# Kernel tuning notes

Measured on AMD Instinct MI355X. Metric: run time of the kernel, lower is better.

## Reference

```python
import jax, jax.numpy as jnp
import numpy as np

B, N_KERNELS, IN_DIM, UNITS = 512, 128, 1024, 1024

def setup_inputs() -> dict:
    key = jax.random.key(0)
    k1, k2 = jax.random.split(key)
    x = jax.random.normal(k1, (B, N_KERNELS, IN_DIM), dtype=jnp.float32)
    kernels = jax.random.normal(k2, (N_KERNELS, IN_DIM, UNITS), dtype=jnp.float32) * 0.02
    return {"x": x, "kernels": kernels}

def reference(x, kernels):
    # Original loops over n_kernels doing x[:, i:i+1, :] @ kernels[i] then softplus.
    # Note: the original's K.bias_add return value is discarded, so bias never
    # affects the output; the faithful math has no bias term.
    # Batched GEMM over the position axis k: [B,K,I] x [K,I,O] -> [B,K,O]
    out = jax.nn.softplus(jnp.einsum('bki,kio->bko', x, kernels))
    return out
```

## Files before the change

### kernel.cpp

```cpp
#include <hip/hip_runtime.h>

#define NKER  128
#define INDIM 1024
#define UNITS 1024

typedef __attribute__((ext_vector_type(8)))  short          bf16x8;
typedef __attribute__((ext_vector_type(4)))  float          f32x4;
typedef __attribute__((ext_vector_type(4)))  unsigned short u16x4;
typedef __attribute__((ext_vector_type(8)))  unsigned short u16x8;

__device__ __forceinline__ unsigned short f2bf(float f) {
    return __builtin_bit_cast(unsigned short, static_cast<__bf16>(f));
}

__device__ __forceinline__ int swzidx(int r, int k) {
    return r * 32 + ((((k >> 3) ^ ((r >> 1) & 3)) << 3) | (k & 7));
}

__global__ void __launch_bounds__(256, 2)
dense_local(const float* __restrict__ X, const float* __restrict__ Kn,
            float* __restrict__ Out)
{
    __shared__ __align__(16) unsigned short lA[2][128 * 32];
    __shared__ __align__(16) unsigned short lB[2][128 * 32];

    const int bid  = blockIdx.x;
    const int wg   = (bid & 7) * 512 + (bid >> 3);
    const int kidx = wg >> 5;
    const int tile = wg & 31;
    const int mt   = tile >> 3;
    const int nt   = tile & 7;

    const int t  = threadIdx.x;
    const int l  = t & 63;
    const int w  = t >> 6;
    const int wr = w >> 1, wc = w & 1;
    const int l15 = l & 15, g = l >> 4;

    const size_t MROW = (size_t)NKER * INDIM;

    const float* Abase = X  + (size_t)mt * 128 * MROW + (size_t)kidx * INDIM;
    const float* Bbase = Kn + (size_t)kidx * INDIM * UNITS + nt * 128;
    float*       Cbase = Out + (size_t)mt * 128 * MROW + (size_t)kidx * UNITS + nt * 128;

    const int ar0 = t >> 3;
    const int akq = (t & 7) << 2;
    const int bn  = ((w & 1) << 6) | l;
    const int bkh = w >> 1;

    f32x4 acc[4][4];
#pragma unroll
    for (int mi = 0; mi < 4; ++mi)
#pragma unroll
        for (int ni = 0; ni < 4; ++ni)
            acc[mi][ni] = f32x4{0.f, 0.f, 0.f, 0.f};

    f32x4 av[4];
    float bv[16];

    auto loadg = [&](int kc) {
#pragma unroll
        for (int p = 0; p < 4; ++p)
            av[p] = *(const f32x4*)(Abase + (size_t)(ar0 + p * 32) * MROW + kc + akq);
        const float* bp = Bbase + (size_t)(kc + bkh * 16) * UNITS + bn;
#pragma unroll
        for (int j = 0; j < 16; ++j)
            bv[j] = bp[(size_t)j * UNITS];
    };

    auto writes = [&](int bb) {
#pragma unroll
        for (int p = 0; p < 4; ++p) {
            const int row = ar0 + p * 32;
            u16x4 h;
#pragma unroll
            for (int c = 0; c < 4; ++c) h[c] = f2bf(av[p][c]);
            *(u16x4*)&lA[bb][swzidx(row, akq)] = h;
        }
        u16x8 h0, h1;
#pragma unroll
        for (int j = 0; j < 8; ++j) { h0[j] = f2bf(bv[j]); h1[j] = f2bf(bv[j + 8]); }
        *(u16x8*)&lB[bb][swzidx(bn, bkh * 16)]     = h0;
        *(u16x8*)&lB[bb][swzidx(bn, bkh * 16 + 8)] = h1;
    };

    auto compute = [&](int bb) {
        bf16x8 af[4], bfr[4];
#pragma unroll
        for (int mi = 0; mi < 4; ++mi) {
            const int r = wr * 64 + mi * 16 + l15;
            af[mi] = *(const bf16x8*)&lA[bb][swzidx(r, g * 8)];
        }
#pragma unroll
        for (int ni = 0; ni < 4; ++ni) {
            const int r = wc * 64 + ni * 16 + l15;
            bfr[ni] = *(const bf16x8*)&lB[bb][swzidx(r, g * 8)];
        }
#pragma unroll
        for (int mi = 0; mi < 4; ++mi)
#pragma unroll
            for (int ni = 0; ni < 4; ++ni)
                acc[mi][ni] = __builtin_amdgcn_mfma_f32_16x16x32_bf16(
                    af[mi], bfr[ni], acc[mi][ni], 0, 0, 0);
    };

    loadg(0);
    writes(0);
    __syncthreads();

    int bb = 0;
#pragma unroll 1
    for (int step = 0; step < 32; ++step) {
        if (step < 31) loadg((step + 1) * 32);
        compute(bb);
        __syncthreads();
        if (step < 31) writes(bb ^ 1);
        __syncthreads();
        bb ^= 1;
    }

#pragma unroll
    for (int mi = 0; mi < 4; ++mi) {
#pragma unroll
        for (int ni = 0; ni < 4; ++ni) {
            const int n = wc * 64 + ni * 16 + l15;
#pragma unroll
            for (int r = 0; r < 4; ++r) {
                const int m = wr * 64 + mi * 16 + g * 4 + r;
                const float v  = acc[mi][ni][r];
                const float sp = fmaxf(v, 0.0f) + log1pf(__expf(-fabsf(v)));
                Cbase[(size_t)m * MROW + n] = sp;
            }
        }
    }
}

extern "C" void kernel_launch(void* const* d_in, const int* in_sizes, int n_in,
                              void* d_out, int out_size, void* d_ws, size_t ws_size,
                              hipStream_t stream) {
    const float* X  = (const float*)d_in[0];
    const float* Kn = (const float*)d_in[1];
    float* O = (float*)d_out;
    dense_local<<<4096, 256, 0, stream>>>(X, Kn, O);
}
```

Measured before the change: 408.0 us.

## Stream A tile to LDS via direct global_load_lds and convert at fragment read

The fp32 A tile now goes straight from global memory into LDS with global_load_lds (XOR-swizzled by column group). It is converted to bf16 only when fragments are read, so register staging and the convert-and-store pass for A disappear. B conversion uses a cheaper rounding pack via perm, and the main loop is unrolled by two with one barrier per half. It also raises launch bounds to 3 waves-per-SIMD occupancy and adds setprio around the MFMA block. The trade-off is doubled LDS for A (fp32 storage) and extra conversion ALU in the compute phase, with possible occupancy limits from LDS size.

```diff
diff --git a/kernel.cpp b/kernel.cpp
--- a/kernel.cpp
+++ b/kernel.cpp
@@ -4,25 +4,31 @@
 #define INDIM 1024
 #define UNITS 1024
 
-typedef __attribute__((ext_vector_type(8)))  short          bf16x8;
-typedef __attribute__((ext_vector_type(4)))  float          f32x4;
-typedef __attribute__((ext_vector_type(4)))  unsigned short u16x4;
-typedef __attribute__((ext_vector_type(8)))  unsigned short u16x8;
+typedef __attribute__((ext_vector_type(8))) short          bf16x8;
+typedef __attribute__((ext_vector_type(4))) float          f32x4;
+typedef __attribute__((ext_vector_type(4))) unsigned int   u32x4;
 
-__device__ __forceinline__ unsigned short f2bf(float f) {
-    return __builtin_bit_cast(unsigned short, static_cast<__bf16>(f));
+typedef __attribute__((address_space(1))) const unsigned int gas_t;
+typedef __attribute__((address_space(3)))       unsigned int las_t;
+#define GLOAD16(g, l) \
+    __builtin_amdgcn_global_load_lds((gas_t*)(g), (las_t*)(l), 16, 0, 0)
+
+__device__ __forceinline__ unsigned int bpack2(float lo, float hi) {
+    unsigned int ul = __builtin_bit_cast(unsigned int, lo) + 0x8000u;
+    unsigned int uh = __builtin_bit_cast(unsigned int, hi) + 0x8000u;
+    return __builtin_amdgcn_perm(uh, ul, 0x07060302u);
 }
 
 __device__ __forceinline__ int swzidx(int r, int k) {
     return r * 32 + ((((k >> 3) ^ ((r >> 1) & 3)) << 3) | (k & 7));
 }
 
-__global__ void __launch_bounds__(256, 2)
+__global__ void __launch_bounds__(256, 3)
 dense_local(const float* __restrict__ X, const float* __restrict__ Kn,
             float* __restrict__ Out)
 {
-    __shared__ __align__(16) unsigned short lA[2][128 * 32];
-    __shared__ __align__(16) unsigned short lB[2][128 * 32];
+    __shared__ __align__(16) float          lAf[2][128 * 32];
+    __shared__ __align__(16) unsigned short lB [2][128 * 32];
 
     const int bid  = blockIdx.x;
     const int wg   = (bid & 7) * 512 + (bid >> 3);
@@ -31,22 +37,26 @@
     const int mt   = tile >> 3;
     const int nt   = tile & 7;
 
-    const int t  = threadIdx.x;
-    const int l  = t & 63;
-    const int w  = t >> 6;
-    const int wr = w >> 1, wc = w & 1;
+    const int t   = threadIdx.x;
+    const int l   = t & 63;
+    const int w   = t >> 6;
+    const int wr  = w >> 1, wc = w & 1;
     const int l15 = l & 15, g = l >> 4;
 
     const size_t MROW = (size_t)NKER * INDIM;
 
-    const float* Abase = X  + (size_t)mt * 128 * MROW + (size_t)kidx * INDIM;
-    const float* Bbase = Kn + (size_t)kidx * INDIM * UNITS + nt * 128;
+    const float* Abase = X   + (size_t)mt * 128 * MROW + (size_t)kidx * INDIM;
+    const float* Bbase = Kn  + (size_t)kidx * INDIM * UNITS + nt * 128;
     float*       Cbase = Out + (size_t)mt * 128 * MROW + (size_t)kidx * UNITS + nt * 128;
 
-    const int ar0 = t >> 3;
-    const int akq = (t & 7) << 2;
+    const int  rlo  = (t >> 3) & 7;
+    const int  cgl  = (t & 7) ^ rlo;
+    const float* aG = Abase + (size_t)(w * 32 + rlo) * MROW + cgl * 4;
+    const size_t MR8 = (size_t)8 * MROW;
+
     const int bn  = ((w & 1) << 6) | l;
     const int bkh = w >> 1;
+    const float* bG = Bbase + (size_t)(bkh * 16) * UNITS + bn;
 
     f32x4 acc[4][4];
 #pragma unroll
@@ -55,68 +65,72 @@
         for (int ni = 0; ni < 4; ++ni)
             acc[mi][ni] = f32x4{0.f, 0.f, 0.f, 0.f};
 
-    f32x4 av[4];
     float bv[16];
 
-    auto loadg = [&](int kc) {
-#pragma unroll
-        for (int p = 0; p < 4; ++p)
-            av[p] = *(const f32x4*)(Abase + (size_t)(ar0 + p * 32) * MROW + kc + akq);
-        const float* bp = Bbase + (size_t)(kc + bkh * 16) * UNITS + bn;
+    auto gloadA = [&](int nb) {
+        GLOAD16(aG,            &lAf[nb][(w * 4 + 0) * 256]);
+        GLOAD16(aG + MR8,      &lAf[nb][(w * 4 + 1) * 256]);
+        GLOAD16(aG + 2 * MR8,  &lAf[nb][(w * 4 + 2) * 256]);
+        GLOAD16(aG + 3 * MR8,  &lAf[nb][(w * 4 + 3) * 256]);
+        aG += 32;
+    };
+    auto loadB = [&]() {
 #pragma unroll
         for (int j = 0; j < 16; ++j)
-            bv[j] = bp[(size_t)j * UNITS];
+            bv[j] = bG[(size_t)j * UNITS];
+        bG += (size_t)32 * UNITS;
+    };
+    auto writeB = [&](int nb) {
+        u32x4 W0{bpack2(bv[0], bv[1]),  bpack2(bv[2], bv[3]),
+                 bpack2(bv[4], bv[5]),  bpack2(bv[6], bv[7])};
+        u32x4 W1{bpack2(bv[8], bv[9]),  bpack2(bv[10], bv[11]),
+                 bpack2(bv[12], bv[13]), bpack2(bv[14], bv[15])};
+        *(u32x4*)&lB[nb][swzidx(bn, bkh * 16)]     = W0;
+        *(u32x4*)&lB[nb][swzidx(bn, bkh * 16 + 8)] = W1;
     };
 
-    auto writes = [&](int bb) {
-#pragma unroll
-        for (int p = 0; p < 4; ++p) {
-            const int row = ar0 + p * 32;
-            u16x4 h;
-#pragma unroll
-            for (int c = 0; c < 4; ++c) h[c] = f2bf(av[p][c]);
-            *(u16x4*)&lA[bb][swzidx(row, akq)] = h;
-        }
-        u16x8 h0, h1;
-#pragma unroll
-        for (int j = 0; j < 8; ++j) { h0[j] = f2bf(bv[j]); h1[j] = f2bf(bv[j + 8]); }
-        *(u16x8*)&lB[bb][swzidx(bn, bkh * 16)]     = h0;
-        *(u16x8*)&lB[bb][swzidx(bn, bkh * 16 + 8)] = h1;
-    };
-
-    auto compute = [&](int bb) {
+    auto compute = [&](int c) {
         bf16x8 af[4], bfr[4];
 #pragma unroll
         for (int mi = 0; mi < 4; ++mi) {
-            const int r = wr * 64 + mi * 16 + l15;
-            af[mi] = *(const bf16x8*)&lA[bb][swzidx(r, g * 8)];
+            const int arow = wr * 64 + mi * 16 + l15;
+            const int ax   = l15 & 7;
+            const float* pa = &lAf[c][arow * 32];
+            f32x4 v0 = *(const f32x4*)(pa + ((( 2 * g)      ^ ax) << 2));
+            f32x4 v1 = *(const f32x4*)(pa + (((2 * g + 1)   ^ ax) << 2));
+            u32x4 pw{bpack2(v0[0], v0[1]), bpack2(v0[2], v0[3]),
+                     bpack2(v1[0], v1[1]), bpack2(v1[2], v1[3])};
+            af[mi] = __builtin_bit_cast(bf16x8, pw);
         }
 #pragma unroll
-        for (int ni = 0; ni < 4; ++ni) {
-            const int r = wc * 64 + ni * 16 + l15;
-            bfr[ni] = *(const bf16x8*)&lB[bb][swzidx(r, g * 8)];
-        }
+        for (int ni = 0; ni < 4; ++ni)
+            bfr[ni] = *(const bf16x8*)&lB[c][swzidx(wc * 64 + ni * 16 + l15, g * 8)];
+        __builtin_amdgcn_s_setprio(1);
 #pragma unroll
         for (int mi = 0; mi < 4; ++mi)
 #pragma unroll
             for (int ni = 0; ni < 4; ++ni)
                 acc[mi][ni] = __builtin_amdgcn_mfma_f32_16x16x32_bf16(
                     af[mi], bfr[ni], acc[mi][ni], 0, 0, 0);
+        __builtin_amdgcn_s_setprio(0);
     };
 
-    loadg(0);
-    writes(0);
+    gloadA(0);
+    loadB();
+    writeB(0);
     __syncthreads();
 
-    int bb = 0;
 #pragma unroll 1
-    for (int step = 0; step < 32; ++step) {
-        if (step < 31) loadg((step + 1) * 32);
-        compute(bb);
+    for (int it = 0; it < 16; ++it) {
+        gloadA(1);
+        loadB();
+        compute(0);
+        writeB(1);
         __syncthreads();
-        if (step < 31) writes(bb ^ 1);
+        if (it < 15) { gloadA(0); loadB(); }
+        compute(1);
+        if (it < 15) writeB(0);
         __syncthreads();
-        bb ^= 1;
     }
 
 #pragma unroll
```

Measured after the change: 450.9 us. +10.5%, slower.
